# Performance work log

Measured on AMD Instinct MI355X. Metric: run time of the kernel, lower is better.

## Reference

```python
import jax, jax.numpy as jnp
import numpy as np

B, T, V = 64, 2048, 512  # batch, max sequence length, vocab_size


def setup_inputs() -> dict:
    key = jax.random.key(0)
    k1, k2, k3, k4 = jax.random.split(key, 4)
    # times: increasing event times (unused by the model's math, but a forward arg)
    times = jnp.cumsum(jax.random.uniform(k1, (B, T), dtype=jnp.float32), axis=1)
    # codes: sparse binary multi-hot code occurrences per visit
    codes = (jax.random.uniform(k2, (B, T, V)) < 0.05).astype(jnp.float32)
    # lengths in [2, T]; force max length = T so padded output width T-1 matches
    # the original's max(lengths)-1
    lengths = jax.random.randint(k3, (B,), 2, T + 1, dtype=jnp.int32)
    lengths = lengths.at[0].set(T)
    # nn.Linear(V, V): xavier_uniform weight, zero bias
    limit = float(np.sqrt(6.0 / (V + V)))
    W = jax.random.uniform(k4, (V, V), minval=-limit, maxval=limit, dtype=jnp.float32)
    b = jnp.zeros((V,), dtype=jnp.float32)
    return {"times": times, "codes": codes, "lengths": lengths, "W": W, "b": b}


def reference(times, codes, lengths, W, b):
    # Prediction k (k = 1..seq_len-1) uses clamp(sum of first k code vectors, 0, 1),
    # i.e. cumsum index k-1. So valid prefix states are cumsum[:, :T-1].
    cum = jnp.clip(jnp.cumsum(codes, axis=1), 0.0, 1.0)[:, :-1]  # [B, T-1, V]
    # Single batched GEMM replacing B*T tiny per-vector Linear calls
    logits = jnp.einsum('btv,uv->btu', cum, W) + b  # [B, T-1, V]
    # Position j is valid iff j < lengths[b] - 1 (patients with len < 2 get all zeros)
    mask = jnp.arange(cum.shape[1])[None, :] < (lengths[:, None] - 1)  # [B, T-1]
    return jnp.where(mask[:, :, None], logits, 0.0)
```

## Files before the change

### kernel.cpp

```cpp
#include <hip/hip_runtime.h>
#include <stdint.h>

#define BB 64
#define TT 2048
#define VV 512
#define TOUT 2047
#define NCH 32
#define CH 64
#define NEARLY 8
#define EV 8

typedef unsigned long long ull;
typedef float f32x2 __attribute__((ext_vector_type(2)));
typedef float f32x4 __attribute__((ext_vector_type(4)));


__global__ void k_transpose(const float* __restrict__ W, float* __restrict__ wT) {
  __shared__ float tile[32][33];
  int bx = blockIdx.x, by = blockIdx.y;
  int tx = threadIdx.x, ty = threadIdx.y;
#pragma unroll
  for (int i = 0; i < 4; ++i)
    tile[ty + i * 8][tx] = W[(size_t)(by * 32 + ty + i * 8) * VV + bx * 32 + tx];
  __syncthreads();
#pragma unroll
  for (int i = 0; i < 4; ++i)
    wT[(size_t)(bx * 32 + ty + i * 8) * VV + by * 32 + tx] = tile[tx][ty + i * 8];
}

__global__ void k_rowsum(const float* __restrict__ W, const float* __restrict__ bias,
                         float* __restrict__ S) {
  int u = blockIdx.x;
  int l = threadIdx.x;
  const float* row = W + (size_t)u * VV;
  float4 a = *(const float4*)(row + 4 * l);
  float4 c = *(const float4*)(row + 256 + 4 * l);
  float s = a.x + a.y + a.z + a.w + c.x + c.y + c.z + c.w;
#pragma unroll
  for (int off = 32; off; off >>= 1) s += __shfl_xor(s, off, 64);
  if (l == 0) S[u] = bias[u] + s;
}

__global__ void k_maskpass(const float* __restrict__ codes, const int* __restrict__ lengths,
                           uint32_t* __restrict__ stashw, ull* __restrict__ chmask,
                           uint32_t* __restrict__ tcopy) {
  int b = blockIdx.y;
  int sub = blockIdx.x;
  int tid = threadIdx.x, lane = tid & 63, w = tid >> 6;
  int validB = min(lengths[b] - 1, TOUT);
  int tstart = sub * 16 + w * 4;
  int n = min(4, validB - tstart);
  ull o0 = 0, o1 = 0, o2 = 0, o3 = 0, o4 = 0, o5 = 0, o6 = 0, o7 = 0;
  int ww = lane & 15, rep = lane >> 4, s = ww >> 1;
  if (n > 0) {
    const float* cp0 = codes + ((size_t)b * TT + tstart) * VV;
    uint32_t* sp0 = stashw + (size_t)(b * TOUT + tstart) * VV + rep * 128 + ww;
    f32x4 fa[4], fb[4];
#pragma unroll
    for (int j = 0; j < 4; ++j)
      if (j < n) {
        const float* cp = cp0 + (size_t)j * VV;
        fa[j] = __builtin_nontemporal_load((const f32x4*)(cp + 4 * lane));
        fb[j] = __builtin_nontemporal_load((const f32x4*)(cp + 256 + 4 * lane));
      }
#pragma unroll
    for (int j = 0; j < 4; ++j)
      if (j < n) {
        ull b0 = __ballot(fa[j][0] != 0.f);
        ull b1 = __ballot(fa[j][1] != 0.f);
        ull b2 = __ballot(fa[j][2] != 0.f);
        ull b3 = __ballot(fa[j][3] != 0.f);
        ull b4 = __ballot(fb[j][0] != 0.f);
        ull b5 = __ballot(fb[j][1] != 0.f);
        ull b6 = __ballot(fb[j][2] != 0.f);
        ull b7 = __ballot(fb[j][3] != 0.f);
        o0 |= b0; o1 |= b1; o2 |= b2; o3 |= b3;
        o4 |= b4; o5 |= b5; o6 |= b6; o7 |= b7;
        ull m01 = (s & 1) ? b1 : b0;
        ull m23 = (s & 1) ? b3 : b2;
        ull m45 = (s & 1) ? b5 : b4;
        ull m67 = (s & 1) ? b7 : b6;
        ull m03 = (s & 2) ? m23 : m01;
        ull m47 = (s & 2) ? m67 : m45;
        ull mm = (s & 4) ? m47 : m03;
        uint32_t val = (ww & 1) ? (uint32_t)(mm >> 32) : (uint32_t)mm;
        sp0[(size_t)j * VV] = val;
        if (rep == 0 && sub < 4)
          tcopy[((size_t)b * 64 + tstart + j) * 16 + ww] = val;
      }
  }
  __shared__ ull red[4][8];
  if (lane == 0) {
    red[w][0] = o0; red[w][1] = o1; red[w][2] = o2; red[w][3] = o3;
    red[w][4] = o4; red[w][5] = o5; red[w][6] = o6; red[w][7] = o7;
  }
  __syncthreads();
  if (tid < 8) {
    ull m = red[0][tid] | red[1][tid] | red[2][tid] | red[3][tid];
    if (m) atomicOr(&chmask[((size_t)b * NCH + (sub >> 2)) * 8 + tid], m);
  }
}

__device__ __forceinline__ int decode_v(int w, int k) {
  return ((w >> 3) << 8) | ((w & 1) << 7) | (k << 2) | ((w >> 1) & 3);
}
__device__ __forceinline__ int dec64(int s, int k) {
  return ((s >> 2) << 8) | (k << 2) | (s & 3);
}

__device__ __forceinline__ void add_bits4(uint32_t bits, int ww, int col,
                                          const float* __restrict__ wT,
                                          f32x2& L) {
#pragma unroll 1
  while (bits) {
    int k0 = __ffs(bits) - 1; bits &= bits - 1;
    int k1 = -1, k2 = -1, k3 = -1;
    if (bits) { k1 = __ffs(bits) - 1; bits &= bits - 1; }
    if (bits) { k2 = __ffs(bits) - 1; bits &= bits - 1; }
    if (bits) { k3 = __ffs(bits) - 1; bits &= bits - 1; }
    f32x2 f0 = *(const f32x2*)(wT + (size_t)decode_v(ww, k0) * VV + col);
    f32x2 acc = f0;
    if (k1 >= 0) { f32x2 f1 = *(const f32x2*)(wT + (size_t)decode_v(ww, k1) * VV + col);
                   acc += f1; }
    if (k2 >= 0) { f32x2 f2 = *(const f32x2*)(wT + (size_t)decode_v(ww, k2) * VV + col);
                   acc += f2; }
    if (k3 >= 0) { f32x2 f3 = *(const f32x2*)(wT + (size_t)decode_v(ww, k3) * VV + col);
                   acc += f3; }
    L += acc;
  }
}

__device__ __forceinline__ void build_bs(uint32_t wreg, ull* bs) {
#pragma unroll
  for (int s2 = 0; s2 < 8; ++s2) {
    uint32_t lo = (uint32_t)__shfl((int)wreg, 2 * s2, 64);
    uint32_t hi = (uint32_t)__shfl((int)wreg, 2 * s2 + 1, 64);
    bs[s2] = ((ull)hi << 32) | lo;
  }
}

__device__ __forceinline__ void accum_bitset(const ull* bs, int col,
                                             const float* __restrict__ wT,
                                             float sign, f32x2& L) {
  f32x2 a0 = {0.f, 0.f}, a1 = {0.f, 0.f}, a2 = {0.f, 0.f}, a3 = {0.f, 0.f};
  int s = 0;
  ull cur = bs[0];
#define NEXT(vk)                                        \
  do {                                                  \
    while (cur == 0 && s < 7) { ++s; cur = bs[s]; }     \
    if (cur) { int kk = __ffsll(cur) - 1; cur &= cur - 1; vk = dec64(s, kk); } \
  } while (0)
  for (;;) {
    int v0 = -1, v1 = -1, v2 = -1, v3 = -1, v4 = -1, v5 = -1, v6 = -1, v7 = -1;
    NEXT(v0); NEXT(v1); NEXT(v2); NEXT(v3);
    NEXT(v4); NEXT(v5); NEXT(v6); NEXT(v7);
    if (v0 < 0) break;
    f32x2 f0, f1, f2, f3, f4, f5, f6, f7;
    f0 = *(const f32x2*)(wT + (size_t)v0 * VV + col);
    if (v1 >= 0) f1 = *(const f32x2*)(wT + (size_t)v1 * VV + col);
    if (v2 >= 0) f2 = *(const f32x2*)(wT + (size_t)v2 * VV + col);
    if (v3 >= 0) f3 = *(const f32x2*)(wT + (size_t)v3 * VV + col);
    if (v4 >= 0) f4 = *(const f32x2*)(wT + (size_t)v4 * VV + col);
    if (v5 >= 0) f5 = *(const f32x2*)(wT + (size_t)v5 * VV + col);
    if (v6 >= 0) f6 = *(const f32x2*)(wT + (size_t)v6 * VV + col);
    if (v7 >= 0) f7 = *(const f32x2*)(wT + (size_t)v7 * VV + col);
    a0 += f0;
    if (v1 >= 0) a1 += f1;
    if (v2 >= 0) a2 += f2;
    if (v3 >= 0) a3 += f3;
    if (v4 >= 0) a0 += f4;
    if (v5 >= 0) a1 += f5;
    if (v6 >= 0) a2 += f6;
    if (v7 >= 0) a3 += f7;
    if (v7 < 0) break;
  }
#undef NEXT
  f32x2 t = (a0 + a1) + (a2 + a3);
  L += sign * t;
}

__global__ void k_scan(const float* __restrict__ wT, const float* __restrict__ S,
                       const float* __restrict__ bias, const int* __restrict__ lengths,
                       float* __restrict__ outw, const uint32_t* __restrict__ stashr,
                       const ull* __restrict__ chmask, const uint32_t* __restrict__ tcopy) {
  int b = blockIdx.y;
  int x = blockIdx.x;
  int tid = threadIdx.x, lane = tid & 63, w = tid >> 6;
  int col = w * 128 + 2 * lane;
  int myw = lane & 15;
  int validB = min(lengths[b] - 1, TOUT);
  bool early = (x < NEARLY);
  int t0, t1;
  if (early) { t0 = x * EV; t1 = t0 + EV; }
  else {
    int sw = (x - NEARLY) + (b % 31);
    if (sw >= 31) sw -= 31;
    t0 = (1 + sw) * CH; t1 = min(t0 + CH, TOUT);
  }
  int pe = min(t1, validB);

  if (t0 < pe) {
    uint32_t Pw = 0;
    if (early) {
      const uint32_t* tc = tcopy + (size_t)b * 64 * 16 + myw;
      uint32_t q0 = 0, q1 = 0, q2 = 0, q3 = 0, q4 = 0, q5 = 0, q6 = 0, q7 = 0;
      int t = 0;
      for (; t + 8 <= t0; t += 8) {
        q0 |= tc[(t + 0) * 16]; q1 |= tc[(t + 1) * 16];
        q2 |= tc[(t + 2) * 16]; q3 |= tc[(t + 3) * 16];
        q4 |= tc[(t + 4) * 16]; q5 |= tc[(t + 5) * 16];
        q6 |= tc[(t + 6) * 16]; q7 |= tc[(t + 7) * 16];
      }
      for (; t < t0; ++t) q0 |= tc[t * 16];
      Pw = (q0 | q1) | (q2 | q3) | ((q4 | q5) | (q6 | q7));
    } else {
      const uint32_t* cm = (const uint32_t*)chmask + (size_t)b * NCH * 16 + myw;
      int cend = t0 / CH;
      uint32_t p0 = 0, p1 = 0, p2 = 0, p3 = 0;
      int cc = 0;
      for (; cc + 4 <= cend; cc += 4) {
        p0 |= cm[(cc + 0) * 16]; p1 |= cm[(cc + 1) * 16];
        p2 |= cm[(cc + 2) * 16]; p3 |= cm[(cc + 3) * 16];
      }
      for (; cc < cend; ++cc) p0 |= cm[cc * 16];
      Pw = p0 | p1 | p2 | p3;
    }
    ull bs[8];
    build_bs(Pw, bs);
    int pc = 0;
#pragma unroll
    for (int s2 = 0; s2 < 8; ++s2) pc += __popcll(bs[s2]);
    bool direct = (pc <= 256);
    f32x2 L;
    if (direct) {
      L[0] = bias[col]; L[1] = bias[col + 1];
      accum_bitset(bs, col, wT, 1.f, L);
    } else {
      L[0] = S[col]; L[1] = S[col + 1];
      ull nb[8];
#pragma unroll
      for (int s2 = 0; s2 < 8; ++s2) nb[s2] = ~bs[s2];
      accum_bitset(nb, col, wT, -1.f, L);
    }

    float* ob = outw + (size_t)b * TOUT * VV + col;
    if (early) {
      const uint32_t* tc = tcopy + (size_t)b * 64 * 16 + myw;
      int n = pe - t0;
      uint32_t vm[EV];
#pragma unroll
      for (int i = 0; i < EV; ++i)
        if (i < n) vm[i] = tc[(t0 + i) * 16];
#pragma unroll 1
      for (int i = 0; i < n; ++i) {
        uint32_t cand = vm[i] & ~Pw;
        uint32_t wwm = (uint32_t)__ballot(cand != 0) & 0xFFFFu;
        Pw |= cand;
        while (wwm) {
          int ww = __ffs(wwm) - 1; wwm &= wwm - 1;
          uint32_t nbw = (uint32_t)__shfl((int)cand, ww, 64);
          add_bits4(nbw, ww, col, wT, L);
        }
        __builtin_nontemporal_store(L, (f32x2*)(ob + (size_t)(t0 + i) * VV));
      }
    } else {
      const uint32_t* stash = stashr + (size_t)b * TOUT * VV + w * 128 + myw;
      int nfull = (pe - t0) >> 4;
      uint32_t vmr[16], vmn[16];
      if (nfull > 0) {
#pragma unroll
        for (int i = 0; i < 16; ++i) vmr[i] = stash[(size_t)(t0 + i) * VV];
      }
#pragma unroll 1
      for (int ib = 0; ib < nfull; ++ib) {
        int base = t0 + ib * 16;
        if (ib + 1 < nfull) {
#pragma unroll
          for (int i = 0; i < 16; ++i) vmn[i] = stash[(size_t)(base + 16 + i) * VV];
        }
#pragma unroll
        for (int i = 0; i < 16; ++i) {
          uint32_t cand = vmr[i] & ~Pw;
          uint32_t wwm = (uint32_t)__ballot(cand != 0) & 0xFFFFu;
          Pw |= cand;
          while (wwm) {
            int ww = __ffs(wwm) - 1; wwm &= wwm - 1;
            uint32_t nbw = (uint32_t)__shfl((int)cand, ww, 64);
            add_bits4(nbw, ww, col, wT, L);
          }
          __builtin_nontemporal_store(L, (f32x2*)(ob + (size_t)(base + i) * VV));
        }
#pragma unroll
        for (int i = 0; i < 16; ++i) vmr[i] = vmn[i];
      }
#pragma unroll 1
      for (int t = t0 + nfull * 16; t < pe; ++t) {
        uint32_t cand = stash[(size_t)t * VV] & ~Pw;
        uint32_t wwm = (uint32_t)__ballot(cand != 0) & 0xFFFFu;
        Pw |= cand;
        while (wwm) {
          int ww = __ffs(wwm) - 1; wwm &= wwm - 1;
          uint32_t nbw = (uint32_t)__shfl((int)cand, ww, 64);
          add_bits4(nbw, ww, col, wT, L);
        }
        __builtin_nontemporal_store(L, (f32x2*)(ob + (size_t)t * VV));
      }
    }
  }
  int z0 = max(t0, validB);
  if (z0 < t1) {
    size_t basep = (size_t)(b * TOUT + z0) * VV;
    size_t n = (size_t)(t1 - z0) * VV;
    f32x4 z = {0.f, 0.f, 0.f, 0.f};
    for (size_t i = (size_t)tid * 4; i < n; i += 256 * 4)
      __builtin_nontemporal_store(z, (f32x4*)(outw + basep + i));
  }
}

extern "C" void kernel_launch(void* const* d_in, const int* in_sizes, int n_in,
                              void* d_out, int out_size, void* d_ws, size_t ws_size,
                              hipStream_t stream) {
  char* times_scratch = (char*)d_in[0];
  float* codes = (float*)d_in[1];
  const int* lengths = (const int*)d_in[2];
  const float* W = (const float*)d_in[3];
  const float* bias = (const float*)d_in[4];
  float* out = (float*)d_out;

  ull* chmask = (ull*)times_scratch;
  float* S = (float*)(times_scratch + 131072);
  uint32_t* tcopy = (uint32_t*)(times_scratch + 135168);
  float* wT = codes;

  hipMemsetAsync(chmask, 0, 128 * 1024, stream);
  k_maskpass<<<dim3(128, BB), dim3(256), 0, stream>>>(codes, lengths,
                                                      (uint32_t*)out, chmask, tcopy);
  k_transpose<<<dim3(16, 16), dim3(32, 8), 0, stream>>>(W, wT);
  k_rowsum<<<dim3(512), dim3(64), 0, stream>>>(W, bias, S);
  k_scan<<<dim3(NEARLY + 31, BB), dim3(256), 0, stream>>>(wT, S, bias, lengths,
                                                          out, (const uint32_t*)out,
                                                          chmask, tcopy);
}
```

Baseline: 483.2 us.

## Halve scan block to 128 threads with four output columns per lane

The scan kernel now runs 2 waves per block instead of 4. Each lane owns 4 contiguous output columns and uses 16-byte vector loads of transposed W rows and 16-byte stores. The mask pass now writes stash words only for the two 256-column halves the new layout reads. This cuts the per-wave bit decoding, ballot and shuffle overhead, which was repeated for every 128 columns, and issues fewer but wider memory operations. The cost is fewer waves per block and less latency hiding per block.

Result: no change. 474.8 us (-1.8%).

```diff
diff --git a/kernel.cpp b/kernel.cpp
--- a/kernel.cpp
+++ b/kernel.cpp
@@ -51,10 +51,11 @@
   int tstart = sub * 16 + w * 4;
   int n = min(4, validB - tstart);
   ull o0 = 0, o1 = 0, o2 = 0, o3 = 0, o4 = 0, o5 = 0, o6 = 0, o7 = 0;
-  int ww = lane & 15, rep = lane >> 4, s = ww >> 1;
+  int ww = lane & 15, s = ww >> 1;
+  int rep2 = (lane >> 4) * 2;
   if (n > 0) {
     const float* cp0 = codes + ((size_t)b * TT + tstart) * VV;
-    uint32_t* sp0 = stashw + (size_t)(b * TOUT + tstart) * VV + rep * 128 + ww;
+    uint32_t* sp0 = stashw + (size_t)(b * TOUT + tstart) * VV + rep2 * 128 + ww;
     f32x4 fa[4], fb[4];
 #pragma unroll
     for (int j = 0; j < 4; ++j)
@@ -84,8 +85,8 @@
         ull m47 = (s & 2) ? m67 : m45;
         ull mm = (s & 4) ? m47 : m03;
         uint32_t val = (ww & 1) ? (uint32_t)(mm >> 32) : (uint32_t)mm;
-        sp0[(size_t)j * VV] = val;
-        if (rep == 0 && sub < 4)
+        if (lane < 32) sp0[(size_t)j * VV] = val;
+        if (lane < 16 && sub < 4)
           tcopy[((size_t)b * 64 + tstart + j) * 16 + ww] = val;
       }
   }
@@ -110,7 +111,7 @@
 
 __device__ __forceinline__ void add_bits4(uint32_t bits, int ww, int col,
                                           const float* __restrict__ wT,
-                                          f32x2& L) {
+                                          f32x4& L) {
 #pragma unroll 1
   while (bits) {
     int k0 = __ffs(bits) - 1; bits &= bits - 1;
@@ -118,13 +119,13 @@
     if (bits) { k1 = __ffs(bits) - 1; bits &= bits - 1; }
     if (bits) { k2 = __ffs(bits) - 1; bits &= bits - 1; }
     if (bits) { k3 = __ffs(bits) - 1; bits &= bits - 1; }
-    f32x2 f0 = *(const f32x2*)(wT + (size_t)decode_v(ww, k0) * VV + col);
-    f32x2 acc = f0;
-    if (k1 >= 0) { f32x2 f1 = *(const f32x2*)(wT + (size_t)decode_v(ww, k1) * VV + col);
+    f32x4 f0 = *(const f32x4*)(wT + (size_t)decode_v(ww, k0) * VV + col);
+    f32x4 acc = f0;
+    if (k1 >= 0) { f32x4 f1 = *(const f32x4*)(wT + (size_t)decode_v(ww, k1) * VV + col);
                    acc += f1; }
-    if (k2 >= 0) { f32x2 f2 = *(const f32x2*)(wT + (size_t)decode_v(ww, k2) * VV + col);
+    if (k2 >= 0) { f32x4 f2 = *(const f32x4*)(wT + (size_t)decode_v(ww, k2) * VV + col);
                    acc += f2; }
-    if (k3 >= 0) { f32x2 f3 = *(const f32x2*)(wT + (size_t)decode_v(ww, k3) * VV + col);
+    if (k3 >= 0) { f32x4 f3 = *(const f32x4*)(wT + (size_t)decode_v(ww, k3) * VV + col);
                    acc += f3; }
     L += acc;
   }
@@ -141,8 +142,8 @@
 
 __device__ __forceinline__ void accum_bitset(const ull* bs, int col,
                                              const float* __restrict__ wT,
-                                             float sign, f32x2& L) {
-  f32x2 a0 = {0.f, 0.f}, a1 = {0.f, 0.f}, a2 = {0.f, 0.f}, a3 = {0.f, 0.f};
+                                             float sign, f32x4& L) {
+  f32x4 a0 = {0.f, 0.f, 0.f, 0.f}, a1 = a0, a2 = a0, a3 = a0;
   int s = 0;
   ull cur = bs[0];
 #define NEXT(vk)                                        \
@@ -155,15 +156,15 @@
     NEXT(v0); NEXT(v1); NEXT(v2); NEXT(v3);
     NEXT(v4); NEXT(v5); NEXT(v6); NEXT(v7);
     if (v0 < 0) break;
-    f32x2 f0, f1, f2, f3, f4, f5, f6, f7;
-    f0 = *(const f32x2*)(wT + (size_t)v0 * VV + col);
-    if (v1 >= 0) f1 = *(const f32x2*)(wT + (size_t)v1 * VV + col);
-    if (v2 >= 0) f2 = *(const f32x2*)(wT + (size_t)v2 * VV + col);
-    if (v3 >= 0) f3 = *(const f32x2*)(wT + (size_t)v3 * VV + col);
-    if (v4 >= 0) f4 = *(const f32x2*)(wT + (size_t)v4 * VV + col);
-    if (v5 >= 0) f5 = *(const f32x2*)(wT + (size_t)v5 * VV + col);
-    if (v6 >= 0) f6 = *(const f32x2*)(wT + (size_t)v6 * VV + col);
-    if (v7 >= 0) f7 = *(const f32x2*)(wT + (size_t)v7 * VV + col);
+    f32x4 f0, f1, f2, f3, f4, f5, f6, f7;
+    f0 = *(const f32x4*)(wT + (size_t)v0 * VV + col);
+    if (v1 >= 0) f1 = *(const f32x4*)(wT + (size_t)v1 * VV + col);
+    if (v2 >= 0) f2 = *(const f32x4*)(wT + (size_t)v2 * VV + col);
+    if (v3 >= 0) f3 = *(const f32x4*)(wT + (size_t)v3 * VV + col);
+    if (v4 >= 0) f4 = *(const f32x4*)(wT + (size_t)v4 * VV + col);
+    if (v5 >= 0) f5 = *(const f32x4*)(wT + (size_t)v5 * VV + col);
+    if (v6 >= 0) f6 = *(const f32x4*)(wT + (size_t)v6 * VV + col);
+    if (v7 >= 0) f7 = *(const f32x4*)(wT + (size_t)v7 * VV + col);
     a0 += f0;
     if (v1 >= 0) a1 += f1;
     if (v2 >= 0) a2 += f2;
@@ -175,7 +176,7 @@
     if (v7 < 0) break;
   }
 #undef NEXT
-  f32x2 t = (a0 + a1) + (a2 + a3);
+  f32x4 t = (a0 + a1) + (a2 + a3);
   L += sign * t;
 }
 
@@ -186,7 +187,7 @@
   int b = blockIdx.y;
   int x = blockIdx.x;
   int tid = threadIdx.x, lane = tid & 63, w = tid >> 6;
-  int col = w * 128 + 2 * lane;
+  int col = w * 256 + 4 * lane;
   int myw = lane & 15;
   int validB = min(lengths[b] - 1, TOUT);
   bool early = (x < NEARLY);
@@ -231,12 +232,12 @@
 #pragma unroll
     for (int s2 = 0; s2 < 8; ++s2) pc += __popcll(bs[s2]);
     bool direct = (pc <= 256);
-    f32x2 L;
+    f32x4 L;
     if (direct) {
-      L[0] = bias[col]; L[1] = bias[col + 1];
+      L = *(const f32x4*)(bias + col);
       accum_bitset(bs, col, wT, 1.f, L);
     } else {
-      L[0] = S[col]; L[1] = S[col + 1];
+      L = *(const f32x4*)(S + col);
       ull nb[8];
 #pragma unroll
       for (int s2 = 0; s2 < 8; ++s2) nb[s2] = ~bs[s2];
@@ -261,10 +262,10 @@
           uint32_t nbw = (uint32_t)__shfl((int)cand, ww, 64);
           add_bits4(nbw, ww, col, wT, L);
         }
-        __builtin_nontemporal_store(L, (f32x2*)(ob + (size_t)(t0 + i) * VV));
+        __builtin_nontemporal_store(L, (f32x4*)(ob + (size_t)(t0 + i) * VV));
       }
     } else {
-      const uint32_t* stash = stashr + (size_t)b * TOUT * VV + w * 128 + myw;
+      const uint32_t* stash = stashr + (size_t)b * TOUT * VV + w * 256 + myw;
       int nfull = (pe - t0) >> 4;
       uint32_t vmr[16], vmn[16];
       if (nfull > 0) {
@@ -288,7 +289,7 @@
             uint32_t nbw = (uint32_t)__shfl((int)cand, ww, 64);
             add_bits4(nbw, ww, col, wT, L);
           }
-          __builtin_nontemporal_store(L, (f32x2*)(ob + (size_t)(base + i) * VV));
+          __builtin_nontemporal_store(L, (f32x4*)(ob + (size_t)(base + i) * VV));
         }
 #pragma unroll
         for (int i = 0; i < 16; ++i) vmr[i] = vmn[i];
@@ -303,7 +304,7 @@
           uint32_t nbw = (uint32_t)__shfl((int)cand, ww, 64);
           add_bits4(nbw, ww, col, wT, L);
         }
-        __builtin_nontemporal_store(L, (f32x2*)(ob + (size_t)t * VV));
+        __builtin_nontemporal_store(L, (f32x4*)(ob + (size_t)t * VV));
       }
     }
   }
@@ -312,7 +313,7 @@
     size_t basep = (size_t)(b * TOUT + z0) * VV;
     size_t n = (size_t)(t1 - z0) * VV;
     f32x4 z = {0.f, 0.f, 0.f, 0.f};
-    for (size_t i = (size_t)tid * 4; i < n; i += 256 * 4)
+    for (size_t i = (size_t)tid * 4; i < n; i += 128 * 4)
       __builtin_nontemporal_store(z, (f32x4*)(outw + basep + i));
   }
 }
@@ -337,7 +338,7 @@
                                                       (uint32_t*)out, chmask, tcopy);
   k_transpose<<<dim3(16, 16), dim3(32, 8), 0, stream>>>(W, wT);
   k_rowsum<<<dim3(512), dim3(64), 0, stream>>>(W, bias, S);
-  k_scan<<<dim3(NEARLY + 31, BB), dim3(256), 0, stream>>>(wT, S, bias, lengths,
+  k_scan<<<dim3(NEARLY + 31, BB), dim3(128), 0, stream>>>(wT, S, bias, lengths,
                                                           out, (const uint32_t*)out,
                                                           chmask, tcopy);
 }
```
